# Kernel tuning notes

Hardware: AMD Instinct MI355X
Metric: run time of the kernel (lower is better)

## Reference

```python
import jax, jax.numpy as jnp
import numpy as np

B, N, C_IN, C_OUT, H_MLP, STEPS, DEG = 8, 128, 512, 512, 128, 10, 16
E = B * N * DEG  # edges per side


def _seg_mean(v, idx, n):
    s = jax.ops.segment_sum(v, idx, num_segments=n)
    c = jax.ops.segment_sum(jnp.ones((v.shape[0], 1), v.dtype), idx, num_segments=n)
    return s / jnp.maximum(c, 1.0)


def _relconv(x, ei, W1, W2, Wr, br):
    n = x.shape[0]
    src, dst = ei[0], ei[1]
    out1 = _seg_mean((x @ W1)[src], dst, n)  # flow source_to_target, mean aggr
    out2 = _seg_mean((x @ W2)[dst], src, n)  # flow target_to_source, mean aggr
    return x @ Wr + br + out1 + out2


def _gnn(x, ei, p):
    # GNNForEmbedding: 1 RelConv layer, LayerNorm(relu(.)), cat=True, lin=True (eval: dropout off)
    W1, W2, Wr, br, g, b, Fw, Fb = p
    h = jax.nn.relu(_relconv(x, ei, W1, W2, Wr, br))
    mu = h.mean(-1, keepdims=True)
    var = ((h - mu) ** 2).mean(-1, keepdims=True)
    h = (h - mu) / jnp.sqrt(var + 1e-5) * g + b
    return jnp.concatenate([x, h], -1) @ Fw + Fb


def setup_inputs():
    key = jax.random.key(0)
    ks = jax.random.split(key, 20)
    nn_ = B * N

    def randn(k, shape, s=1.0):
        return jax.random.normal(k, shape, jnp.float32) * s

    def mk_edges(k):
        k1, k2 = jax.random.split(k)
        off = jnp.repeat(jnp.arange(B, dtype=jnp.int32) * N, N * DEG)
        src = jax.random.randint(k1, (E,), 0, N, jnp.int32) + off
        dst = jax.random.randint(k2, (E,), 0, N, jnp.int32) + off
        return jnp.stack([src, dst])

    s = 0.04
    inp = {
        'x_s': randn(ks[0], (nn_, C_IN)),
        'edge_index_s': mk_edges(ks[1]),
        'edge_attr_s': randn(ks[2], (E, 1)),
        'batch_s': jnp.repeat(jnp.arange(B, dtype=jnp.int32), N),
        'x_t': randn(ks[3], (nn_, C_IN)),
        'edge_index_t': mk_edges(ks[4]),
        'edge_attr_t': randn(ks[5], (E, 1)),
        'batch_t': jnp.repeat(jnp.arange(B, dtype=jnp.int32), N),
        'e_lin1': randn(ks[6], (C_IN, C_OUT), s),
        'e_lin2': randn(ks[7], (C_IN, C_OUT), s),
        'e_rw': randn(ks[8], (C_IN, C_OUT), s),
        'e_rb': jnp.zeros((C_OUT,), jnp.float32),
        'e_g': jnp.ones((C_OUT,), jnp.float32),
        'e_b': jnp.zeros((C_OUT,), jnp.float32),
        'e_fw': randn(ks[9], (C_IN + C_OUT, C_OUT), s),
        'e_fb': jnp.zeros((C_OUT,), jnp.float32),
        'c_lin1': randn(ks[10], (C_IN, C_OUT), s),
        'c_lin2': randn(ks[11], (C_IN, C_OUT), s),
        'c_rw': randn(ks[12], (C_IN, C_OUT), s),
        'c_rb': jnp.zeros((C_OUT,), jnp.float32),
        'c_g': jnp.ones((C_OUT,), jnp.float32),
        'c_b': jnp.zeros((C_OUT,), jnp.float32),
        'c_fw': randn(ks[13], (C_IN + C_OUT, C_OUT), s),
        'c_fb': jnp.zeros((C_OUT,), jnp.float32),
        'm_w1': randn(ks[14], (C_OUT, H_MLP), s),
        'm_b1': jnp.zeros((H_MLP,), jnp.float32),
        'm_w2': randn(ks[15], (H_MLP,), s),
        'm_b2': jnp.zeros((), jnp.float32),
    }
    return inp


def reference(x_s, edge_index_s, edge_attr_s, batch_s, x_t, edge_index_t, edge_attr_t, batch_t,
              e_lin1, e_lin2, e_rw, e_rb, e_g, e_b, e_fw, e_fb,
              c_lin1, c_lin2, c_rw, c_rb, c_g, c_b, c_fw, c_fb,
              m_w1, m_b1, m_w2, m_b2):
    pe = (e_lin1, e_lin2, e_rw, e_rb, e_g, e_b, e_fw, e_fb)
    pc = (c_lin1, c_lin2, c_rw, c_rb, c_g, c_b, c_fw, c_fb)
    # embedding GNN (detached in original model)
    Hs = jax.lax.stop_gradient(_gnn(x_s, edge_index_s, pe)).reshape(B, N, C_OUT)
    Ht = jax.lax.stop_gradient(_gnn(x_t, edge_index_t, pe)).reshape(B, N, C_OUT)
    # all graphs have exactly N nodes -> masks are all-True, masked_softmax == softmax
    S_hat = jnp.einsum('bsc,btc->bst', Hs, Ht)
    S_0 = jax.nn.softmax(S_hat, axis=-1).reshape(B * N, N)
    rkey = jax.random.key(42)
    for t in range(STEPS):
        S = jax.nn.softmax(S_hat, axis=-1)
        R_s = jax.random.normal(jax.random.fold_in(rkey, t), (B, N, C_IN), jnp.float32)
        R_t = jnp.einsum('bst,bsc->btc', S, R_s)  # S^T @ R_s
        O_s = _gnn(R_s.reshape(-1, C_IN), edge_index_s, pc).reshape(B, N, C_OUT)
        O_t = _gnn(R_t.reshape(-1, C_IN), edge_index_t, pc).reshape(B, N, C_OUT)
        # fc1(O_s_i - O_t_j) = O_s_i@W1 - O_t_j@W1 + b1 (linearity): avoid O(Ns*Nt*C) diff tensor
        A = O_s @ m_w1 + m_b1          # [B, Ns, H]
        Bm = O_t @ m_w1                # [B, Nt, H]
        hid = jax.nn.relu(A[:, :, None, :] - Bm[:, None, :, :])  # [B, Ns, Nt, H]
        S_hat = S_hat + (hid @ m_w2 + m_b2)
    S_L = jax.nn.softmax(S_hat, axis=-1).reshape(B * N, N)
    return (S_0, S_L)
```

## Files before the change

### kernel.cpp

```cpp
#include <hip/hip_runtime.h>
#include <stdint.h>


typedef unsigned short u16;
typedef unsigned int u32;
typedef __attribute__((ext_vector_type(8))) short short8;
typedef __attribute__((ext_vector_type(4))) float f32x4;

__device__ inline u16 f2bf(float x) {
  u32 u = __float_as_uint(x);
  u32 r = (u + 0x7fffu + ((u >> 16) & 1u)) >> 16;
  return (u16)r;
}
__device__ inline float bf2f(u16 h) { return __uint_as_float(((u32)h) << 16); }
__device__ inline void split2(float x, u16& h, u16& l) {
  h = f2bf(x);
  l = f2bf(x - bf2f(h));
}

__host__ __device__ inline void tf2x32(uint32_t k0, uint32_t k1, uint32_t x0,
                                       uint32_t x1, uint32_t& o0, uint32_t& o1) {
  uint32_t ks0 = k0, ks1 = k1, ks2 = 0x1BD11BDAu ^ k0 ^ k1;
  x0 += ks0; x1 += ks1;
#define TF_R(r) { x0 += x1; x1 = (x1 << r) | (x1 >> (32 - r)); x1 ^= x0; }
  TF_R(13) TF_R(15) TF_R(26) TF_R(6)   x0 += ks1; x1 += ks2 + 1u;
  TF_R(17) TF_R(29) TF_R(16) TF_R(24)  x0 += ks2; x1 += ks0 + 2u;
  TF_R(13) TF_R(15) TF_R(26) TF_R(6)   x0 += ks0; x1 += ks1 + 3u;
  TF_R(17) TF_R(29) TF_R(16) TF_R(24)  x0 += ks1; x1 += ks2 + 4u;
  TF_R(13) TF_R(15) TF_R(26) TF_R(6)   x0 += ks2; x1 += ks0 + 5u;
#undef TF_R
  o0 = x0; o1 = x1;
}

__device__ inline float erfinv_f(float x) {
  float w = -log1pf(-x * x);
  float p;
  if (w < 5.0f) {
    w = w - 2.5f;
    p = 2.81022636e-08f;
    p = fmaf(p, w, 3.43273939e-07f);
    p = fmaf(p, w, -3.5233877e-06f);
    p = fmaf(p, w, -4.39150654e-06f);
    p = fmaf(p, w, 0.00021858087f);
    p = fmaf(p, w, -0.00125372503f);
    p = fmaf(p, w, -0.00417768164f);
    p = fmaf(p, w, 0.246640727f);
    p = fmaf(p, w, 1.50140941f);
  } else {
    w = sqrtf(w) - 3.0f;
    p = -0.000200214257f;
    p = fmaf(p, w, 0.000100950558f);
    p = fmaf(p, w, 0.00134934322f);
    p = fmaf(p, w, -0.00367342844f);
    p = fmaf(p, w, 0.00573950773f);
    p = fmaf(p, w, -0.0076224613f);
    p = fmaf(p, w, 0.00943887047f);
    p = fmaf(p, w, 1.00167406f);
    p = fmaf(p, w, 2.83297682f);
  }
  return p * x;
}

__device__ inline float bits_to_normal(uint32_t bits) {
  uint32_t fb = (bits >> 9) | 0x3f800000u;
  float f = __uint_as_float(fb) - 1.0f;
  float u = f * 2.0f + (-0.99999994f);
  u = fmaxf(-0.99999994f, u);
  return 1.41421356f * erfinv_f(u);
}

template <int OUTP, int BIASN, int BIASM, int AGGB>
__global__ __launch_bounds__(256) void mfma_gemm(
    int K,
    const u16* __restrict__ Ah, const u16* __restrict__ Al, int lda, int sA,
    const u16* __restrict__ Bh, const u16* __restrict__ Bl, int ldb, int sB,
    float* __restrict__ Cf, u16* __restrict__ Ch, u16* __restrict__ Cl,
    int ldc, int sC, const float* __restrict__ bias) {
  const int g = blockIdx.z;
  Ah += (size_t)g * sA; Al += (size_t)g * sA;
  Bh += (size_t)g * sB; Bl += (size_t)g * sB;
  if (OUTP) { Ch += (size_t)g * sC; Cl += (size_t)g * sC; }
  else { Cf += (size_t)g * sC; }
  __shared__ u16 As[2][64][64];
  __shared__ u16 Bs[2][64][64];
  const int tid = threadIdx.x;
  const int m0 = blockIdx.y * 64, n0 = blockIdx.x * 64;
  const int l = tid & 63;
  const int w = tid >> 6;
  const int wr = (w >> 1) * 32, wc = (w & 1) * 32;
  const int l15 = l & 15, lq = l >> 4;
  f32x4 acc[2][2] = {};
  const int sr = tid >> 3, sc = tid & 7;
  for (int k0 = 0; k0 < K; k0 += 64) {
    __syncthreads();
#pragma unroll
    for (int p = 0; p < 2; ++p) {
      int r = sr + p * 32;
      int dst = (sc ^ (r & 7)) * 8;
      *(uint4*)&As[0][r][dst] = *(const uint4*)&Ah[(size_t)(m0 + r) * lda + k0 + sc * 8];
      *(uint4*)&As[1][r][dst] = *(const uint4*)&Al[(size_t)(m0 + r) * lda + k0 + sc * 8];
      size_t boff;
      if (AGGB) {
        int rowg = (k0 < 128) ? (n0 + r) : (512 + n0 + r);
        boff = (size_t)rowg * ldb + (k0 & 127) + sc * 8;
      } else {
        boff = (size_t)(n0 + r) * ldb + k0 + sc * 8;
      }
      *(uint4*)&Bs[0][r][dst] = *(const uint4*)&Bh[boff];
      *(uint4*)&Bs[1][r][dst] = *(const uint4*)&Bl[boff];
    }
    __syncthreads();
#pragma unroll
    for (int kk = 0; kk < 2; ++kk) {
      short8 aH[2], aL[2], bH[2], bL[2];
#pragma unroll
      for (int i = 0; i < 2; ++i) {
        int mr = wr + i * 16 + l15;
        int ca = ((kk * 4 + lq) ^ (mr & 7)) * 8;
        aH[i] = *(const short8*)&As[0][mr][ca];
        aL[i] = *(const short8*)&As[1][mr][ca];
        int nr = wc + i * 16 + l15;
        int cb = ((kk * 4 + lq) ^ (nr & 7)) * 8;
        bH[i] = *(const short8*)&Bs[0][nr][cb];
        bL[i] = *(const short8*)&Bs[1][nr][cb];
      }
#pragma unroll
      for (int i = 0; i < 2; ++i)
#pragma unroll
        for (int j = 0; j < 2; ++j) {
          acc[i][j] = __builtin_amdgcn_mfma_f32_16x16x32_bf16(aH[i], bH[j], acc[i][j], 0, 0, 0);
          acc[i][j] = __builtin_amdgcn_mfma_f32_16x16x32_bf16(aL[i], bH[j], acc[i][j], 0, 0, 0);
          acc[i][j] = __builtin_amdgcn_mfma_f32_16x16x32_bf16(aH[i], bL[j], acc[i][j], 0, 0, 0);
        }
    }
  }
#pragma unroll
  for (int i = 0; i < 2; ++i)
#pragma unroll
    for (int j = 0; j < 2; ++j) {
      int n = n0 + wc + j * 16 + l15;
      int mb = m0 + wr + i * 16 + lq * 4;
      f32x4 v = acc[i][j];
      if (BIASN) {
        float b = bias[n];
        v[0] += b; v[1] += b; v[2] += b; v[3] += b;
      }
      if (BIASM) {
        f32x4 bb = *(const f32x4*)&bias[mb];
        v[0] += bb[0]; v[1] += bb[1]; v[2] += bb[2]; v[3] += bb[3];
      }
      if (OUTP) {
        u16 h[4], lo[4];
        split2(v[0], h[0], lo[0]); split2(v[1], h[1], lo[1]);
        split2(v[2], h[2], lo[2]); split2(v[3], h[3], lo[3]);
        uint2 hv = {(u32)h[0] | ((u32)h[1] << 16), (u32)h[2] | ((u32)h[3] << 16)};
        uint2 lv = {(u32)lo[0] | ((u32)lo[1] << 16), (u32)lo[2] | ((u32)lo[3] << 16)};
        *(uint2*)&Ch[(size_t)n * ldc + mb] = hv;
        *(uint2*)&Cl[(size_t)n * ldc + mb] = lv;
      } else {
        *(f32x4*)&Cf[(size_t)n * ldc + mb] = v;
      }
    }
}

__global__ __launch_bounds__(256) void count_kernel(const int* __restrict__ ei_s,
                                                    const int* __restrict__ ei_t,
                                                    int* __restrict__ Acnt,
                                                    int* __restrict__ degd,
                                                    int* __restrict__ degs) {
  int e = blockIdx.x * 256 + threadIdx.x;
  int side = e >> 14, idx = e & 16383;
  const int* ei = side ? ei_t : ei_s;
  int src = ei[idx], dst = ei[16384 + idx];
  int g = (dst >> 7) + side * 8;
  int dl = dst & 127, sl = src & 127;
  atomicAdd(&Acnt[(g * 128 + dl) * 128 + sl], 1);
  atomicAdd(&degd[g * 128 + dl], 1);
  atomicAdd(&degs[g * 128 + sl], 1);
}

__global__ __launch_bounds__(256) void norm_adj_kernel(const int* __restrict__ Acnt,
                                                       const int* __restrict__ degd,
                                                       const int* __restrict__ degs,
                                                       u16* __restrict__ Mh,
                                                       u16* __restrict__ Ml) {
  int idx = blockIdx.x * 256 + threadIdx.x;
  int g = idx >> 15, m = (idx >> 8) & 127, k = idx & 255;
  float val;
  if (k < 128)
    val = (float)Acnt[(g * 128 + m) * 128 + k] / (float)max(degd[g * 128 + m], 1);
  else
    val = (float)Acnt[(g * 128 + (k - 128)) * 128 + m] / (float)max(degs[g * 128 + m], 1);
  u16 h, lo;
  split2(val, h, lo);
  Mh[idx] = h; Ml[idx] = lo;
}

__global__ __launch_bounds__(256) void pack_kernel(const float* __restrict__ W1,
                                                   const float* __restrict__ W2,
                                                   const float* __restrict__ Wr,
                                                   float* __restrict__ Wcat) {
  int idx = blockIdx.x * 256 + threadIdx.x;
  int k = idx / 384, j4 = (idx % 384) * 4;
  float4 v;
  if (j4 < 512)       v = *(const float4*)&W1[k * 512 + j4];
  else if (j4 < 1024) v = *(const float4*)&W2[k * 512 + j4 - 512];
  else                v = *(const float4*)&Wr[k * 512 + j4 - 1024];
  *(float4*)&Wcat[k * 1536 + j4] = v;
}

__global__ __launch_bounds__(256) void convert_wT(const float* __restrict__ W,
                                                  u16* __restrict__ Th,
                                                  u16* __restrict__ Tl,
                                                  int K, int N) {
  int id = blockIdx.x * 256 + threadIdx.x;
  int k = id / N, n = id - k * N;
  u16 h, lo;
  split2(W[id], h, lo);
  Th[n * K + k] = h;
  Tl[n * K + k] = lo;
}

__global__ __launch_bounds__(128) void fbm_kernel(const float* __restrict__ fb,
                                                  const float* __restrict__ w1,
                                                  const float* __restrict__ b1,
                                                  float* __restrict__ fbm) {
  int h = threadIdx.x;
  float acc = b1[h];
  for (int c = 0; c < 512; ++c) acc = fmaf(fb[c], w1[c * 128 + h], acc);
  fbm[h] = acc;
}

__global__ __launch_bounds__(256) void copyx_kernel(const float* __restrict__ xs,
                                                    const float* __restrict__ xt,
                                                    u16* __restrict__ XHh,
                                                    u16* __restrict__ XHl) {
  int idx = blockIdx.x * 256 + threadIdx.x;
  int row = idx >> 7, c4 = (idx & 127) << 2;
  const float* src = (row < 1024) ? (xs + row * 512 + c4)
                                  : (xt + (row - 1024) * 512 + c4);
  float4 v = *(const float4*)src;
  u16 h[4], lo[4];
  split2(v.x, h[0], lo[0]); split2(v.y, h[1], lo[1]);
  split2(v.z, h[2], lo[2]); split2(v.w, h[3], lo[3]);
  uint2 hv = {(u32)h[0] | ((u32)h[1] << 16), (u32)h[2] | ((u32)h[3] << 16)};
  uint2 lv = {(u32)lo[0] | ((u32)lo[1] << 16), (u32)lo[2] | ((u32)lo[3] << 16)};
  *(uint2*)&XHh[row * 1024 + c4] = hv;
  *(uint2*)&XHl[row * 1024 + c4] = lv;
}

__global__ __launch_bounds__(256) void gemm_f32(
    int M, int N, int K,
    const float* __restrict__ A, int lda,
    const float* __restrict__ B, int ldb,
    float* __restrict__ C, int ldc) {
  int m0 = blockIdx.y * 64, n0 = blockIdx.x * 64;
  __shared__ float As[16][64];
  __shared__ float Bs[16][64];
  int tid = threadIdx.x;
  int tx = tid & 15, ty = tid >> 4;
  float acc[4][4] = {};
  for (int k0 = 0; k0 < K; k0 += 16) {
    {
      int m_l = tid & 63, k_l = (tid >> 6) << 2;
      float4 av = *(const float4*)&A[(m0 + m_l) * lda + k0 + k_l];
      As[k_l + 0][m_l] = av.x; As[k_l + 1][m_l] = av.y;
      As[k_l + 2][m_l] = av.z; As[k_l + 3][m_l] = av.w;
    }
    {
      int k_l = tid >> 4, n_l = (tid & 15) << 2;
      float4 bv = *(const float4*)&B[(k0 + k_l) * ldb + n0 + n_l];
      *(float4*)&Bs[k_l][n_l] = bv;
    }
    __syncthreads();
#pragma unroll
    for (int kk = 0; kk < 16; ++kk) {
      float4 a4 = *(const float4*)&As[kk][ty << 2];
      float4 b4 = *(const float4*)&Bs[kk][tx << 2];
      float av[4] = {a4.x, a4.y, a4.z, a4.w};
      float bv[4] = {b4.x, b4.y, b4.z, b4.w};
#pragma unroll
      for (int i = 0; i < 4; ++i)
#pragma unroll
        for (int j = 0; j < 4; ++j) acc[i][j] = fmaf(av[i], bv[j], acc[i][j]);
    }
    __syncthreads();
  }
#pragma unroll
  for (int i = 0; i < 4; ++i) {
    int m = m0 + (ty << 2) + i;
    float4 v = {acc[i][0], acc[i][1], acc[i][2], acc[i][3]};
    *(float4*)&C[m * ldc + n0 + (tx << 2)] = v;
  }
}

__global__ __launch_bounds__(256) void ln_stats(
    const u16* __restrict__ Yth, const u16* __restrict__ Ytl,
    const float* __restrict__ AGGt, const float* __restrict__ rb,
    float* __restrict__ partS, float* __restrict__ partQ) {
  int cg = blockIdx.x, ng = blockIdx.y;
  int lane = threadIdx.x & 63, cs = threadIdx.x >> 6;
  int node = ng * 64 + lane;
  float s = 0.f, q = 0.f;
#pragma unroll
  for (int k = 0; k < 16; ++k) {
    int c = cg * 64 + cs * 16 + k;
    size_t yi = (size_t)(1024 + c) * 2048 + node;
    float v = bf2f(Yth[yi]) + bf2f(Ytl[yi]) + rb[c] + AGGt[(size_t)c * 2048 + node];
    v = fmaxf(v, 0.f);
    s += v; q += v * v;
  }
  __shared__ float ls[4][64], lq[4][64];
  ls[cs][lane] = s; lq[cs][lane] = q;
  __syncthreads();
  if (cs == 0) {
    s = ls[0][lane] + ls[1][lane] + ls[2][lane] + ls[3][lane];
    q = lq[0][lane] + lq[1][lane] + lq[2][lane] + lq[3][lane];
    partS[cg * 2048 + node] = s;
    partQ[cg * 2048 + node] = q;
  }
}

__global__ __launch_bounds__(256) void ln_apply(
    const u16* __restrict__ Yth, const u16* __restrict__ Ytl,
    const float* __restrict__ AGGt, const float* __restrict__ partS,
    const float* __restrict__ partQ, const float* __restrict__ rb,
    const float* __restrict__ gam, const float* __restrict__ bet,
    u16* __restrict__ XHh, u16* __restrict__ XHl) {
  int cg = blockIdx.x, ng = blockIdx.y;
  int lane = threadIdx.x & 63, cs = threadIdx.x >> 6;
  int node = ng * 64 + lane;
  float s = 0.f, q = 0.f;
#pragma unroll
  for (int p = 0; p < 8; ++p) {
    s += partS[p * 2048 + node];
    q += partQ[p * 2048 + node];
  }
  float mu = s * (1.f / 512.f);
  float var = q * (1.f / 512.f) - mu * mu;
  float inv = 1.f / sqrtf(var + 1e-5f);
  __shared__ u16 oth[64][66], otl[64][66];
#pragma unroll
  for (int k = 0; k < 16; ++k) {
    int c = cg * 64 + cs * 16 + k;
    size_t yi = (size_t)(1024 + c) * 2048 + node;
    float v = bf2f(Yth[yi]) + bf2f(Ytl[yi]) + rb[c] + AGGt[(size_t)c * 2048 + node];
    v = fmaxf(v, 0.f);
    float o = (v - mu) * inv * gam[c] + bet[c];
    u16 h, lo;
    split2(o, h, lo);
    oth[lane][cs * 16 + k] = h;
    otl[lane][cs * 16 + k] = lo;
  }
  __syncthreads();
  int nl = threadIdx.x >> 2, cq = (threadIdx.x & 3) * 16;
  size_t xbase = (size_t)(ng * 64 + nl) * 1024 + 512 + cg * 64 + cq;
  uint4 h0, h1, l0, l1;
  h0 = *(const uint4*)&oth[nl][cq];     h1 = *(const uint4*)&oth[nl][cq + 8];
  l0 = *(const uint4*)&otl[nl][cq];     l1 = *(const uint4*)&otl[nl][cq + 8];
  *(uint4*)&XHh[xbase] = h0;  *(uint4*)&XHh[xbase + 8] = h1;
  *(uint4*)&XHl[xbase] = l0;  *(uint4*)&XHl[xbase + 8] = l1;
}

__global__ __launch_bounds__(256) void srk_kernel(
    const float* __restrict__ SH, u16* __restrict__ STh, u16* __restrict__ STl,
    u16* __restrict__ RsTh, u16* __restrict__ RsTl,
    u16* __restrict__ XHh, u16* __restrict__ XHl,
    float* __restrict__ outp, u32 k0, u32 k1) {
  int bid = blockIdx.x;
  int tid = threadIdx.x;
  if (bid < 512) {
    int r = bid * 2 + (tid >> 7);
    int t = tid & 127;
    int gg = r >> 7, s = r & 127;
    float a = SH[r * 128 + t];
    float m = a;
#pragma unroll
    for (int off = 32; off > 0; off >>= 1) m = fmaxf(m, __shfl_xor(m, off));
    __shared__ float red[2][4];
    int wv = tid >> 6;
    if ((tid & 63) == 0) red[0][wv] = m;
    __syncthreads();
    m = fmaxf(red[0][wv], red[0][wv ^ 1]);
    float e = expf(a - m);
    float su = e;
#pragma unroll
    for (int off = 32; off > 0; off >>= 1) su += __shfl_xor(su, off);
    if ((tid & 63) == 0) red[1][wv] = su;
    __syncthreads();
    su = red[1][wv] + red[1][wv ^ 1];
    float p = e / su;
    u16 h, lo;
    split2(p, h, lo);
    STh[(gg * 128 + t) * 128 + s] = h;
    STl[(gg * 128 + t) * 128 + s] = lo;
    if (outp) outp[r * 128 + t] = p;
  } else {
    u32 j = (u32)(bid - 512) * 256 + tid;
    u32 o0, o1;
    tf2x32(k0, k1, 0u, j, o0, o1);
    float val = bits_to_normal(o0 ^ o1);
    u32 node = j >> 9, ch = j & 511;
    u16 h, lo;
    split2(val, h, lo);
    XHh[node * 1024 + ch] = h;
    XHl[node * 1024 + ch] = lo;
    RsTh[ch * 1024 + node] = h;
    RsTl[ch * 1024 + node] = lo;
  }
}

__global__ __launch_bounds__(128) void dist_kernel(const float* __restrict__ Pt,
                                                   const float* __restrict__ b1,
                                                   const float* __restrict__ w2,
                                                   const float* __restrict__ b2,
                                                   float* __restrict__ SH) {
  int bs = blockIdx.x;
  int gb = bs >> 7;
  int t = threadIdx.x;
  __shared__ float arow[128], w2s[128];
  arow[t] = Pt[(size_t)t * 2048 + bs] + b1[t];
  w2s[t] = w2[t];
  __syncthreads();
  const float* pt = Pt + 1024 + gb * 128 + t;
  float acc = 0.f;
#pragma unroll 8
  for (int h = 0; h < 128; ++h) {
    float pv = pt[(size_t)h * 2048];
    acc += fmaxf(arow[h] - pv, 0.f) * w2s[h];
  }
  SH[bs * 128 + t] += acc + b2[0];
}

extern "C" void kernel_launch(void* const* d_in, const int* in_sizes, int n_in,
                              void* d_out, int out_size, void* d_ws, size_t ws_size,
                              hipStream_t stream) {
  const float* x_s = (const float*)d_in[0];
  const int* ei_s = (const int*)d_in[1];
  const float* x_t = (const float*)d_in[4];
  const int* ei_t = (const int*)d_in[5];
  const float* e_lin1 = (const float*)d_in[8];
  const float* e_lin2 = (const float*)d_in[9];
  const float* e_rw = (const float*)d_in[10];
  const float* e_rb = (const float*)d_in[11];
  const float* e_g = (const float*)d_in[12];
  const float* e_b = (const float*)d_in[13];
  const float* e_fw = (const float*)d_in[14];
  const float* e_fb = (const float*)d_in[15];
  const float* c_lin1 = (const float*)d_in[16];
  const float* c_lin2 = (const float*)d_in[17];
  const float* c_rw = (const float*)d_in[18];
  const float* c_rb = (const float*)d_in[19];
  const float* c_g = (const float*)d_in[20];
  const float* c_b = (const float*)d_in[21];
  const float* c_fw = (const float*)d_in[22];
  const float* c_fb = (const float*)d_in[23];
  const float* m_w1 = (const float*)d_in[24];
  const float* m_b1 = (const float*)d_in[25];
  const float* m_w2 = (const float*)d_in[26];
  const float* m_b2 = (const float*)d_in[27];
  float* out = (float*)d_out;
  float* ws = (float*)d_ws;

  u16* Mch   = (u16*)(ws + 0);
  u16* Mcl   = (u16*)(ws + 262144);
  u16* Yth   = (u16*)(ws + 524288);
  u16* Ytl   = (u16*)(ws + 2097152);
  float* AGGt = ws + 3670016;
  float* Pt   = AGGt;
  u16* XHh   = (u16*)(ws + 4718592);
  u16* XHl   = (u16*)(ws + 5767168);
  u16* WTeh  = (u16*)(ws + 6815744);
  u16* WTel  = (u16*)(ws + 7208960);
  u16* WTch  = (u16*)(ws + 7602176);
  u16* WTcl  = (u16*)(ws + 7995392);
  u16* FTeh  = (u16*)(ws + 8388608);
  u16* FTel  = (u16*)(ws + 8650752);
  u16* FmTh  = (u16*)(ws + 8912896);
  u16* FmTl  = (u16*)(ws + 8978432);
  u16* Oh    = (u16*)(ws + 9043968);
  u16* Ol    = (u16*)(ws + 9568256);
  u16* RsTh  = (u16*)(ws + 10092544);
  u16* RsTl  = (u16*)(ws + 10354688);
  u16* STh   = (u16*)(ws + 10616832);
  u16* STl   = (u16*)(ws + 10682368);
  float* SH  = ws + 10747904;
  float* Wstage = ws + 10878976;
  float* fbm = ws + 11665408;
  float* partS = ws + 11665536;
  float* partQ = ws + 11681920;
  int* Acnt  = (int*)Yth;
  int* degd  = Acnt + 262144;
  int* degs  = degd + 2048;

  hipMemsetAsync(Acnt, 0, (262144 + 4096) * sizeof(int), stream);
  count_kernel<<<128, 256, 0, stream>>>(ei_s, ei_t, Acnt, degd, degs);
  norm_adj_kernel<<<2048, 256, 0, stream>>>(Acnt, degd, degs, Mch, Mcl);
  pack_kernel<<<768, 256, 0, stream>>>(e_lin1, e_lin2, e_rw, Wstage);
  convert_wT<<<3072, 256, 0, stream>>>(Wstage, WTeh, WTel, 512, 1536);
  pack_kernel<<<768, 256, 0, stream>>>(c_lin1, c_lin2, c_rw, Wstage);
  convert_wT<<<3072, 256, 0, stream>>>(Wstage, WTch, WTcl, 512, 1536);
  convert_wT<<<2048, 256, 0, stream>>>(e_fw, FTeh, FTel, 1024, 512);
  gemm_f32<<<dim3(2, 16, 1), 256, 0, stream>>>(1024, 128, 512, c_fw, 512,
                                               m_w1, 128, Wstage, 128);
  convert_wT<<<512, 256, 0, stream>>>(Wstage, FmTh, FmTl, 1024, 128);
  fbm_kernel<<<1, 128, 0, stream>>>(c_fb, m_w1, m_b1, fbm);
  copyx_kernel<<<1024, 256, 0, stream>>>(x_s, x_t, XHh, XHl);

  auto relu_ln = [&](const float* rb, const float* g, const float* bb) {
    ln_stats<<<dim3(8, 32), 256, 0, stream>>>(Yth, Ytl, AGGt, rb, partS, partQ);
    ln_apply<<<dim3(8, 32), 256, 0, stream>>>(Yth, Ytl, AGGt, partS, partQ,
                                              rb, g, bb, XHh, XHl);
  };

  mfma_gemm<1, 0, 0, 0><<<dim3(24, 32, 1), 256, 0, stream>>>(
      512, XHh, XHl, 1024, 0, WTeh, WTel, 512, 0,
      nullptr, Yth, Ytl, 2048, 0, nullptr);
  mfma_gemm<0, 0, 0, 1><<<dim3(8, 2, 16), 256, 0, stream>>>(
      256, Mch, Mcl, 256, 32768, Yth, Ytl, 2048, 128,
      AGGt, nullptr, nullptr, 2048, 128, nullptr);
  relu_ln(e_rb, e_g, e_b);
  mfma_gemm<1, 0, 1, 0><<<dim3(32, 8, 1), 256, 0, stream>>>(
      1024, FTeh, FTel, 1024, 0, XHh, XHl, 1024, 0,
      nullptr, Oh, Ol, 512, 0, e_fb);
  mfma_gemm<0, 0, 0, 0><<<dim3(2, 2, 8), 256, 0, stream>>>(
      512, Oh + 1024 * 512, Ol + 1024 * 512, 512, 128 * 512,
      Oh, Ol, 512, 128 * 512,
      SH, nullptr, nullptr, 128, 16384, nullptr);

  for (int t = 0; t < 10; ++t) {
    uint32_t fk0, fk1;
    tf2x32(0u, 42u, 0u, (uint32_t)t, fk0, fk1);
    srk_kernel<<<2560, 256, 0, stream>>>(SH, STh, STl, RsTh, RsTl, XHh, XHl,
                                         (t == 0) ? out : nullptr, fk0, fk1);
    mfma_gemm<1, 0, 0, 0><<<dim3(2, 8, 8), 256, 0, stream>>>(
        128, RsTh, RsTl, 1024, 128, STh, STl, 128, 16384,
        nullptr, XHh + 1024 * 1024, XHl + 1024 * 1024, 1024, 128 * 1024, nullptr);
    mfma_gemm<1, 0, 0, 0><<<dim3(24, 32, 1), 256, 0, stream>>>(
        512, XHh, XHl, 1024, 0, WTch, WTcl, 512, 0,
        nullptr, Yth, Ytl, 2048, 0, nullptr);
    mfma_gemm<0, 0, 0, 1><<<dim3(8, 2, 16), 256, 0, stream>>>(
        256, Mch, Mcl, 256, 32768, Yth, Ytl, 2048, 128,
        AGGt, nullptr, nullptr, 2048, 128, nullptr);
    relu_ln(c_rb, c_g, c_b);
    mfma_gemm<0, 1, 0, 0><<<dim3(2, 32, 1), 256, 0, stream>>>(
        1024, XHh, XHl, 1024, 0, FmTh, FmTl, 1024, 0,
        Pt, nullptr, nullptr, 2048, 0, fbm);
    dist_kernel<<<1024, 128, 0, stream>>>(Pt, m_b1, m_w2, m_b2, SH);
  }
  srk_kernel<<<512, 256, 0, stream>>>(SH, STh, STl, RsTh, RsTl, XHh, XHl,
                                      out + 131072, 0u, 0u);
}
```

Measured before the change: 1.023 ms.

## Fuse distance update into softmax/RNG kernel and add 128x128 GEMM tile

Merges the per-step dist_kernel into the following softmax+RNG kernel so the S_hat update, softmax, transpose-split and next-step random generation run in one launch per iteration. This removes a launch and a round trip of SH through memory. It also adds a 512-thread 128x128-tile MFMA GEMM with XOR-swizzled LDS for the large weight GEMMs, giving more reuse per block but fewer blocks, which risks lower occupancy and less spread across CUs.

```diff
diff --git a/kernel.cpp b/kernel.cpp
--- a/kernel.cpp
+++ b/kernel.cpp
@@ -163,6 +163,84 @@
     }
 }
 
+template <int BIASM>
+__global__ __launch_bounds__(512) void mfma_gemm_big(
+    int K,
+    const u16* __restrict__ Ah, const u16* __restrict__ Al, int lda,
+    const u16* __restrict__ Bh, const u16* __restrict__ Bl, int ldb,
+    u16* __restrict__ Ch, u16* __restrict__ Cl, int ldc,
+    const float* __restrict__ bias) {
+  __shared__ u16 As[2][128][64];
+  __shared__ u16 Bs[2][128][64];
+  const int tid = threadIdx.x;
+  const int m0 = blockIdx.y * 128, n0 = blockIdx.x * 128;
+  const int l = tid & 63;
+  const int w = tid >> 6;
+  const int wm = (w >> 2) * 64;
+  const int wn = (w & 3) * 32;
+  const int l15 = l & 15, lq = l >> 4;
+  f32x4 acc[4][2] = {};
+  const int sr = tid >> 3, sc = tid & 7;
+  for (int k0 = 0; k0 < K; k0 += 64) {
+    __syncthreads();
+#pragma unroll
+    for (int p = 0; p < 2; ++p) {
+      int r = p * 64 + sr;
+      int dst = (sc ^ (r & 7)) * 8;
+      *(uint4*)&As[0][r][dst] = *(const uint4*)&Ah[(size_t)(m0 + r) * lda + k0 + sc * 8];
+      *(uint4*)&As[1][r][dst] = *(const uint4*)&Al[(size_t)(m0 + r) * lda + k0 + sc * 8];
+      *(uint4*)&Bs[0][r][dst] = *(const uint4*)&Bh[(size_t)(n0 + r) * ldb + k0 + sc * 8];
+      *(uint4*)&Bs[1][r][dst] = *(const uint4*)&Bl[(size_t)(n0 + r) * ldb + k0 + sc * 8];
+    }
+    __syncthreads();
+#pragma unroll
+    for (int kk = 0; kk < 2; ++kk) {
+      short8 aH[4], aL[4], bH[2], bL[2];
+#pragma unroll
+      for (int i = 0; i < 4; ++i) {
+        int mr = wm + i * 16 + l15;
+        int ca = ((kk * 4 + lq) ^ (mr & 7)) * 8;
+        aH[i] = *(const short8*)&As[0][mr][ca];
+        aL[i] = *(const short8*)&As[1][mr][ca];
+      }
+#pragma unroll
+      for (int j = 0; j < 2; ++j) {
+        int nr = wn + j * 16 + l15;
+        int cb = ((kk * 4 + lq) ^ (nr & 7)) * 8;
+        bH[j] = *(const short8*)&Bs[0][nr][cb];
+        bL[j] = *(const short8*)&Bs[1][nr][cb];
+      }
+#pragma unroll
+      for (int i = 0; i < 4; ++i)
+#pragma unroll
+        for (int j = 0; j < 2; ++j) {
+          acc[i][j] = __builtin_amdgcn_mfma_f32_16x16x32_bf16(aH[i], bH[j], acc[i][j], 0, 0, 0);
+          acc[i][j] = __builtin_amdgcn_mfma_f32_16x16x32_bf16(aL[i], bH[j], acc[i][j], 0, 0, 0);
+          acc[i][j] = __builtin_amdgcn_mfma_f32_16x16x32_bf16(aH[i], bL[j], acc[i][j], 0, 0, 0);
+        }
+    }
+  }
+#pragma unroll
+  for (int i = 0; i < 4; ++i)
+#pragma unroll
+    for (int j = 0; j < 2; ++j) {
+      int n = n0 + wn + j * 16 + l15;
+      int mb = m0 + wm + i * 16 + lq * 4;
+      f32x4 v = acc[i][j];
+      if (BIASM) {
+        f32x4 bb = *(const f32x4*)&bias[mb];
+        v[0] += bb[0]; v[1] += bb[1]; v[2] += bb[2]; v[3] += bb[3];
+      }
+      u16 h[4], lo[4];
+      split2(v[0], h[0], lo[0]); split2(v[1], h[1], lo[1]);
+      split2(v[2], h[2], lo[2]); split2(v[3], h[3], lo[3]);
+      uint2 hv = {(u32)h[0] | ((u32)h[1] << 16), (u32)h[2] | ((u32)h[3] << 16)};
+      uint2 lv = {(u32)lo[0] | ((u32)lo[1] << 16), (u32)lo[2] | ((u32)lo[3] << 16)};
+      *(uint2*)&Ch[(size_t)n * ldc + mb] = hv;
+      *(uint2*)&Cl[(size_t)n * ldc + mb] = lv;
+    }
+}
+
 __global__ __launch_bounds__(256) void count_kernel(const int* __restrict__ ei_s,
                                                     const int* __restrict__ ei_t,
                                                     int* __restrict__ Acnt,
@@ -362,40 +440,59 @@
   *(uint4*)&XHl[xbase] = l0;  *(uint4*)&XHl[xbase + 8] = l1;
 }
 
-__global__ __launch_bounds__(256) void srk_kernel(
-    const float* __restrict__ SH, u16* __restrict__ STh, u16* __restrict__ STl,
+__global__ __launch_bounds__(256) void tail_kernel(
+    float* __restrict__ SH, const float* __restrict__ Pt,
+    const float* __restrict__ b1, const float* __restrict__ w2,
+    const float* __restrict__ b2,
+    u16* __restrict__ STh, u16* __restrict__ STl,
     u16* __restrict__ RsTh, u16* __restrict__ RsTl,
     u16* __restrict__ XHh, u16* __restrict__ XHl,
-    float* __restrict__ outp, u32 k0, u32 k1) {
+    float* __restrict__ outp, int do_rng, u32 k0, u32 k1) {
   int bid = blockIdx.x;
   int tid = threadIdx.x;
   if (bid < 512) {
-    int r = bid * 2 + (tid >> 7);
+    int rl = tid >> 7;
     int t = tid & 127;
-    int gg = r >> 7, s = r & 127;
-    float a = SH[r * 128 + t];
-    float m = a;
+    int bs = bid * 2 + rl;
+    int gg = bs >> 7, s = bs & 127;
+    float val = SH[bs * 128 + t];
+    if (Pt) {
+      __shared__ float arow[2][128], w2s[128];
+      arow[rl][t] = Pt[(size_t)t * 2048 + bs] + b1[t];
+      if (tid < 128) w2s[tid] = w2[tid];
+      __syncthreads();
+      const float* pt = Pt + 1024 + gg * 128 + t;
+      float acc = 0.f;
+#pragma unroll 8
+      for (int h = 0; h < 128; ++h) {
+        float pv = pt[(size_t)h * 2048];
+        acc += fmaxf(arow[rl][h] - pv, 0.f) * w2s[h];
+      }
+      val += acc + b2[0];
+      SH[bs * 128 + t] = val;
+    }
+    float m = val;
 #pragma unroll
     for (int off = 32; off > 0; off >>= 1) m = fmaxf(m, __shfl_xor(m, off));
-    __shared__ float red[2][4];
+    __shared__ float redm[4], reds[4];
     int wv = tid >> 6;
-    if ((tid & 63) == 0) red[0][wv] = m;
-    __syncthreads();
-    m = fmaxf(red[0][wv], red[0][wv ^ 1]);
-    float e = expf(a - m);
+    if ((tid & 63) == 0) redm[wv] = m;
+    __syncthreads();
+    m = fmaxf(redm[wv], redm[wv ^ 1]);
+    float e = expf(val - m);
     float su = e;
 #pragma unroll
     for (int off = 32; off > 0; off >>= 1) su += __shfl_xor(su, off);
-    if ((tid & 63) == 0) red[1][wv] = su;
-    __syncthreads();
-    su = red[1][wv] + red[1][wv ^ 1];
+    if ((tid & 63) == 0) reds[wv] = su;
+    __syncthreads();
+    su = reds[wv] + reds[wv ^ 1];
     float p = e / su;
     u16 h, lo;
     split2(p, h, lo);
     STh[(gg * 128 + t) * 128 + s] = h;
     STl[(gg * 128 + t) * 128 + s] = lo;
-    if (outp) outp[r * 128 + t] = p;
-  } else {
+    if (outp) outp[bs * 128 + t] = p;
+  } else if (do_rng) {
     u32 j = (u32)(bid - 512) * 256 + tid;
     u32 o0, o1;
     tf2x32(k0, k1, 0u, j, o0, o1);
@@ -408,28 +505,6 @@
     RsTh[ch * 1024 + node] = h;
     RsTl[ch * 1024 + node] = lo;
   }
-}
-
-__global__ __launch_bounds__(128) void dist_kernel(const float* __restrict__ Pt,
-                                                   const float* __restrict__ b1,
-                                                   const float* __restrict__ w2,
-                                                   const float* __restrict__ b2,
-                                                   float* __restrict__ SH) {
-  int bs = blockIdx.x;
-  int gb = bs >> 7;
-  int t = threadIdx.x;
-  __shared__ float arow[128], w2s[128];
-  arow[t] = Pt[(size_t)t * 2048 + bs] + b1[t];
-  w2s[t] = w2[t];
-  __syncthreads();
-  const float* pt = Pt + 1024 + gb * 128 + t;
-  float acc = 0.f;
-#pragma unroll 8
-  for (int h = 0; h < 128; ++h) {
-    float pv = pt[(size_t)h * 2048];
-    acc += fmaxf(arow[h] - pv, 0.f) * w2s[h];
-  }
-  SH[bs * 128 + t] += acc + b2[0];
 }
 
 extern "C" void kernel_launch(void* const* d_in, const int* in_sizes, int n_in,
@@ -513,32 +588,33 @@
                                               rb, g, bb, XHh, XHl);
   };
 
-  mfma_gemm<1, 0, 0, 0><<<dim3(24, 32, 1), 256, 0, stream>>>(
-      512, XHh, XHl, 1024, 0, WTeh, WTel, 512, 0,
-      nullptr, Yth, Ytl, 2048, 0, nullptr);
+  mfma_gemm_big<0><<<dim3(12, 16), 512, 0, stream>>>(
+      512, XHh, XHl, 1024, WTeh, WTel, 512, Yth, Ytl, 2048, nullptr);
   mfma_gemm<0, 0, 0, 1><<<dim3(8, 2, 16), 256, 0, stream>>>(
       256, Mch, Mcl, 256, 32768, Yth, Ytl, 2048, 128,
       AGGt, nullptr, nullptr, 2048, 128, nullptr);
   relu_ln(e_rb, e_g, e_b);
-  mfma_gemm<1, 0, 1, 0><<<dim3(32, 8, 1), 256, 0, stream>>>(
-      1024, FTeh, FTel, 1024, 0, XHh, XHl, 1024, 0,
-      nullptr, Oh, Ol, 512, 0, e_fb);
+  mfma_gemm_big<1><<<dim3(16, 4), 512, 0, stream>>>(
+      1024, FTeh, FTel, 1024, XHh, XHl, 1024, Oh, Ol, 512, e_fb);
   mfma_gemm<0, 0, 0, 0><<<dim3(2, 2, 8), 256, 0, stream>>>(
       512, Oh + 1024 * 512, Ol + 1024 * 512, 512, 128 * 512,
       Oh, Ol, 512, 128 * 512,
       SH, nullptr, nullptr, 128, 16384, nullptr);
 
+  {
+    uint32_t fk0, fk1;
+    tf2x32(0u, 42u, 0u, 0u, fk0, fk1);
+    tail_kernel<<<2560, 256, 0, stream>>>(SH, nullptr, m_b1, m_w2, m_b2,
+                                          STh, STl, RsTh, RsTl, XHh, XHl,
+                                          out, 1, fk0, fk1);
+  }
+
   for (int t = 0; t < 10; ++t) {
-    uint32_t fk0, fk1;
-    tf2x32(0u, 42u, 0u, (uint32_t)t, fk0, fk1);
-    srk_kernel<<<2560, 256, 0, stream>>>(SH, STh, STl, RsTh, RsTl, XHh, XHl,
-                                         (t == 0) ? out : nullptr, fk0, fk1);
     mfma_gemm<1, 0, 0, 0><<<dim3(2, 8, 8), 256, 0, stream>>>(
         128, RsTh, RsTl, 1024, 128, STh, STl, 128, 16384,
         nullptr, XHh + 1024 * 1024, XHl + 1024 * 1024, 1024, 128 * 1024, nullptr);
-    mfma_gemm<1, 0, 0, 0><<<dim3(24, 32, 1), 256, 0, stream>>>(
-        512, XHh, XHl, 1024, 0, WTch, WTcl, 512, 0,
-        nullptr, Yth, Ytl, 2048, 0, nullptr);
+    mfma_gemm_big<0><<<dim3(12, 16), 512, 0, stream>>>(
+        512, XHh, XHl, 1024, WTch, WTcl, 512, Yth, Ytl, 2048, nullptr);
     mfma_gemm<0, 0, 0, 1><<<dim3(8, 2, 16), 256, 0, stream>>>(
         256, Mch, Mcl, 256, 32768, Yth, Ytl, 2048, 128,
         AGGt, nullptr, nullptr, 2048, 128, nullptr);
@@ -546,8 +622,11 @@
     mfma_gemm<0, 1, 0, 0><<<dim3(2, 32, 1), 256, 0, stream>>>(
         1024, XHh, XHl, 1024, 0, FmTh, FmTl, 1024, 0,
         Pt, nullptr, nullptr, 2048, 0, fbm);
-    dist_kernel<<<1024, 128, 0, stream>>>(Pt, m_b1, m_w2, m_b2, SH);
-  }
-  srk_kernel<<<512, 256, 0, stream>>>(SH, STh, STl, RsTh, RsTl, XHh, XHl,
-                                      out + 131072, 0u, 0u);
-}
+    uint32_t fk0, fk1;
+    tf2x32(0u, 42u, 0u, (uint32_t)(t + 1), fk0, fk1);
+    int do_rng = (t < 9) ? 1 : 0;
+    tail_kernel<<<do_rng ? 2560 : 512, 256, 0, stream>>>(
+        SH, Pt, m_b1, m_w2, m_b2, STh, STl, RsTh, RsTl, XHh, XHl,
+        (t == 9) ? (out + 131072) : nullptr, do_rng, fk0, fk1);
+  }
+}
```

New measurement: 1.040 ms. Within noise of the previous version (+1.7%).

## Reassociate S^T@R_s through weights and fold Fm projection into main GEMM

Applied to the files above, without the earlier changes.

The R_t = S^T R_s product is now applied after multiplying by the packed weights: R_s is projected through [W1|W2|Wr|Fm_top] once for all nodes, and the result for the target rows is obtained by multiplying S^T with the projected source features. This removes the transposed R_s copy and the separate K=1024 Fm GEMM, whose x-half is now extra output columns of the main GEMM and is added back through a new PADD epilogue. Weight packing and transposition are fused into one kernel, and the random-generation kernel is moved to the end of each iteration. The risk is that the main GEMM now covers only the source half plus extra columns, and the reassociated product changes rounding order slightly.

```diff
diff --git a/kernel.cpp b/kernel.cpp
--- a/kernel.cpp
+++ b/kernel.cpp
@@ -69,13 +69,14 @@
   return 1.41421356f * erfinv_f(u);
 }
 
-template <int OUTP, int BIASN, int BIASM, int AGGB>
+template <int OUTP, int BIASN, int BIASM, int AGGB, int PADD>
 __global__ __launch_bounds__(256) void mfma_gemm(
     int K,
     const u16* __restrict__ Ah, const u16* __restrict__ Al, int lda, int sA,
     const u16* __restrict__ Bh, const u16* __restrict__ Bl, int ldb, int sB,
     float* __restrict__ Cf, u16* __restrict__ Ch, u16* __restrict__ Cl,
-    int ldc, int sC, const float* __restrict__ bias) {
+    int ldc, int sC, const float* __restrict__ bias,
+    const u16* __restrict__ Padh, const u16* __restrict__ Padl) {
   const int g = blockIdx.z;
   Ah += (size_t)g * sA; Al += (size_t)g * sA;
   Bh += (size_t)g * sB; Bl += (size_t)g * sB;
@@ -149,6 +150,14 @@
         f32x4 bb = *(const f32x4*)&bias[mb];
         v[0] += bb[0]; v[1] += bb[1]; v[2] += bb[2]; v[3] += bb[3];
       }
+      if (PADD) {
+        uint2 ph = *(const uint2*)&Padh[(size_t)n * 2048 + mb];
+        uint2 pl = *(const uint2*)&Padl[(size_t)n * 2048 + mb];
+        v[0] += bf2f((u16)(ph.x & 0xffff)) + bf2f((u16)(pl.x & 0xffff));
+        v[1] += bf2f((u16)(ph.x >> 16)) + bf2f((u16)(pl.x >> 16));
+        v[2] += bf2f((u16)(ph.y & 0xffff)) + bf2f((u16)(pl.y & 0xffff));
+        v[3] += bf2f((u16)(ph.y >> 16)) + bf2f((u16)(pl.y >> 16));
+      }
       if (OUTP) {
         u16 h[4], lo[4];
         split2(v[0], h[0], lo[0]); split2(v[1], h[1], lo[1]);
@@ -196,17 +205,18 @@
   Mh[idx] = h; Ml[idx] = lo;
 }
 
-__global__ __launch_bounds__(256) void pack_kernel(const float* __restrict__ W1,
-                                                   const float* __restrict__ W2,
-                                                   const float* __restrict__ Wr,
-                                                   float* __restrict__ Wcat) {
-  int idx = blockIdx.x * 256 + threadIdx.x;
-  int k = idx / 384, j4 = (idx % 384) * 4;
-  float4 v;
-  if (j4 < 512)       v = *(const float4*)&W1[k * 512 + j4];
-  else if (j4 < 1024) v = *(const float4*)&W2[k * 512 + j4 - 512];
-  else                v = *(const float4*)&Wr[k * 512 + j4 - 1024];
-  *(float4*)&Wcat[k * 1536 + j4] = v;
+__global__ __launch_bounds__(256) void convert_packed(const float* __restrict__ W1,
+                                                      const float* __restrict__ W2,
+                                                      const float* __restrict__ Wr,
+                                                      u16* __restrict__ Th,
+                                                      u16* __restrict__ Tl) {
+  int id = blockIdx.x * 256 + threadIdx.x;
+  int n = id >> 9, k = id & 511;
+  const float* W = (n < 512) ? W1 : ((n < 1024) ? W2 : Wr);
+  float v = W[k * 512 + (n & 511)];
+  u16 h, lo;
+  split2(v, h, lo);
+  Th[id] = h; Tl[id] = lo;
 }
 
 __global__ __launch_bounds__(256) void convert_wT(const float* __restrict__ W,
@@ -219,6 +229,25 @@
   split2(W[id], h, lo);
   Th[n * K + k] = h;
   Tl[n * K + k] = lo;
+}
+
+__global__ __launch_bounds__(256) void fm_split(const float* __restrict__ Fm,
+                                                u16* __restrict__ WFTch,
+                                                u16* __restrict__ WFTcl,
+                                                u16* __restrict__ FmTrh,
+                                                u16* __restrict__ FmTrl) {
+  int id = blockIdx.x * 256 + threadIdx.x;
+  int k = id >> 7, h = id & 127;
+  float v = Fm[k * 128 + h];
+  u16 hi, lo;
+  split2(v, hi, lo);
+  if (k < 512) {
+    WFTch[(size_t)(1536 + h) * 512 + k] = hi;
+    WFTcl[(size_t)(1536 + h) * 512 + k] = lo;
+  } else {
+    FmTrh[(size_t)h * 512 + (k - 512)] = hi;
+    FmTrl[(size_t)h * 512 + (k - 512)] = lo;
+  }
 }
 
 __global__ __launch_bounds__(128) void fbm_kernel(const float* __restrict__ fb,
@@ -364,7 +393,6 @@
 
 __global__ __launch_bounds__(256) void srk_kernel(
     const float* __restrict__ SH, u16* __restrict__ STh, u16* __restrict__ STl,
-    u16* __restrict__ RsTh, u16* __restrict__ RsTl,
     u16* __restrict__ XHh, u16* __restrict__ XHl,
     float* __restrict__ outp, u32 k0, u32 k1) {
   int bid = blockIdx.x;
@@ -405,8 +433,6 @@
     split2(val, h, lo);
     XHh[node * 1024 + ch] = h;
     XHl[node * 1024 + ch] = lo;
-    RsTh[ch * 1024 + node] = h;
-    RsTl[ch * 1024 + node] = lo;
   }
 }
 
@@ -465,30 +491,28 @@
   u16* Mch   = (u16*)(ws + 0);
   u16* Mcl   = (u16*)(ws + 262144);
   u16* Yth   = (u16*)(ws + 524288);
-  u16* Ytl   = (u16*)(ws + 2097152);
-  float* AGGt = ws + 3670016;
-  float* Pt   = AGGt;
-  u16* XHh   = (u16*)(ws + 4718592);
-  u16* XHl   = (u16*)(ws + 5767168);
-  u16* WTeh  = (u16*)(ws + 6815744);
-  u16* WTel  = (u16*)(ws + 7208960);
-  u16* WTch  = (u16*)(ws + 7602176);
-  u16* WTcl  = (u16*)(ws + 7995392);
-  u16* FTeh  = (u16*)(ws + 8388608);
-  u16* FTel  = (u16*)(ws + 8650752);
-  u16* FmTh  = (u16*)(ws + 8912896);
-  u16* FmTl  = (u16*)(ws + 8978432);
-  u16* Oh    = (u16*)(ws + 9043968);
-  u16* Ol    = (u16*)(ws + 9568256);
-  u16* RsTh  = (u16*)(ws + 10092544);
-  u16* RsTl  = (u16*)(ws + 10354688);
-  u16* STh   = (u16*)(ws + 10616832);
-  u16* STl   = (u16*)(ws + 10682368);
-  float* SH  = ws + 10747904;
-  float* Wstage = ws + 10878976;
-  float* fbm = ws + 11665408;
-  float* partS = ws + 11665536;
-  float* partQ = ws + 11681920;
+  u16* Ytl   = (u16*)(ws + 2228224);
+  float* AGGt = ws + 3932160;
+  u16* XHh   = (u16*)(ws + 4980736);
+  u16* XHl   = (u16*)(ws + 6029312);
+  u16* WTeh  = (u16*)(ws + 7077888);
+  u16* WTel  = (u16*)(ws + 7471104);
+  u16* WFTch = (u16*)(ws + 7864320);
+  u16* WFTcl = (u16*)(ws + 8290304);
+  u16* FTeh  = (u16*)(ws + 8716288);
+  u16* FTel  = (u16*)(ws + 8978432);
+  u16* FmTrh = (u16*)(ws + 9240576);
+  u16* FmTrl = (u16*)(ws + 9273344);
+  u16* Oh    = (u16*)(ws + 9306112);
+  u16* Ol    = (u16*)(ws + 9830400);
+  u16* STh   = (u16*)(ws + 10354688);
+  u16* STl   = (u16*)(ws + 10420224);
+  float* SH  = ws + 10485760;
+  float* Pt  = ws + 10616832;
+  float* Fm  = ws + 10878976;
+  float* fbm = ws + 11010048;
+  float* partS = ws + 11010176;
+  float* partQ = ws + 11026560;
   int* Acnt  = (int*)Yth;
   int* degd  = Acnt + 262144;
   int* degs  = degd + 2048;
@@ -496,58 +520,59 @@
   hipMemsetAsync(Acnt, 0, (262144 + 4096) * sizeof(int), stream);
   count_kernel<<<128, 256, 0, stream>>>(ei_s, ei_t, Acnt, degd, degs);
   norm_adj_kernel<<<2048, 256, 0, stream>>>(Acnt, degd, degs, Mch, Mcl);
-  pack_kernel<<<768, 256, 0, stream>>>(e_lin1, e_lin2, e_rw, Wstage);
-  convert_wT<<<3072, 256, 0, stream>>>(Wstage, WTeh, WTel, 512, 1536);
-  pack_kernel<<<768, 256, 0, stream>>>(c_lin1, c_lin2, c_rw, Wstage);
-  convert_wT<<<3072, 256, 0, stream>>>(Wstage, WTch, WTcl, 512, 1536);
+  convert_packed<<<3072, 256, 0, stream>>>(e_lin1, e_lin2, e_rw, WTeh, WTel);
+  convert_packed<<<3072, 256, 0, stream>>>(c_lin1, c_lin2, c_rw, WFTch, WFTcl);
   convert_wT<<<2048, 256, 0, stream>>>(e_fw, FTeh, FTel, 1024, 512);
   gemm_f32<<<dim3(2, 16, 1), 256, 0, stream>>>(1024, 128, 512, c_fw, 512,
-                                               m_w1, 128, Wstage, 128);
-  convert_wT<<<512, 256, 0, stream>>>(Wstage, FmTh, FmTl, 1024, 128);
+                                               m_w1, 128, Fm, 128);
+  fm_split<<<512, 256, 0, stream>>>(Fm, WFTch, WFTcl, FmTrh, FmTrl);
   fbm_kernel<<<1, 128, 0, stream>>>(c_fb, m_w1, m_b1, fbm);
   copyx_kernel<<<1024, 256, 0, stream>>>(x_s, x_t, XHh, XHl);
 
-  auto relu_ln = [&](const float* rb, const float* g, const float* bb) {
-    ln_stats<<<dim3(8, 32), 256, 0, stream>>>(Yth, Ytl, AGGt, rb, partS, partQ);
-    ln_apply<<<dim3(8, 32), 256, 0, stream>>>(Yth, Ytl, AGGt, partS, partQ,
-                                              rb, g, bb, XHh, XHl);
-  };
-
-  mfma_gemm<1, 0, 0, 0><<<dim3(24, 32, 1), 256, 0, stream>>>(
+  mfma_gemm<1, 0, 0, 0, 0><<<dim3(24, 32, 1), 256, 0, stream>>>(
       512, XHh, XHl, 1024, 0, WTeh, WTel, 512, 0,
-      nullptr, Yth, Ytl, 2048, 0, nullptr);
-  mfma_gemm<0, 0, 0, 1><<<dim3(8, 2, 16), 256, 0, stream>>>(
+      nullptr, Yth, Ytl, 2048, 0, nullptr, nullptr, nullptr);
+  mfma_gemm<0, 0, 0, 1, 0><<<dim3(8, 2, 16), 256, 0, stream>>>(
       256, Mch, Mcl, 256, 32768, Yth, Ytl, 2048, 128,
-      AGGt, nullptr, nullptr, 2048, 128, nullptr);
-  relu_ln(e_rb, e_g, e_b);
-  mfma_gemm<1, 0, 1, 0><<<dim3(32, 8, 1), 256, 0, stream>>>(
+      AGGt, nullptr, nullptr, 2048, 128, nullptr, nullptr, nullptr);
+  ln_stats<<<dim3(8, 32), 256, 0, stream>>>(Yth, Ytl, AGGt, e_rb, partS, partQ);
+  ln_apply<<<dim3(8, 32), 256, 0, stream>>>(Yth, Ytl, AGGt, partS, partQ,
+                                            e_rb, e_g, e_b, XHh, XHl);
+  mfma_gemm<1, 0, 1, 0, 0><<<dim3(32, 8, 1), 256, 0, stream>>>(
       1024, FTeh, FTel, 1024, 0, XHh, XHl, 1024, 0,
-      nullptr, Oh, Ol, 512, 0, e_fb);
-  mfma_gemm<0, 0, 0, 0><<<dim3(2, 2, 8), 256, 0, stream>>>(
+      nullptr, Oh, Ol, 512, 0, e_fb, nullptr, nullptr);
+  mfma_gemm<0, 0, 0, 0, 0><<<dim3(2, 2, 8), 256, 0, stream>>>(
       512, Oh + 1024 * 512, Ol + 1024 * 512, 512, 128 * 512,
       Oh, Ol, 512, 128 * 512,
-      SH, nullptr, nullptr, 128, 16384, nullptr);
+      SH, nullptr, nullptr, 128, 16384, nullptr, nullptr, nullptr);
+
+  {
+    uint32_t fk0, fk1;
+    tf2x32(0u, 42u, 0u, 0u, fk0, fk1);
+    srk_kernel<<<2560, 256, 0, stream>>>(SH, STh, STl, XHh, XHl, out, fk0, fk1);
+  }
 
   for (int t = 0; t < 10; ++t) {
+    mfma_gemm<1, 0, 0, 0, 0><<<dim3(26, 16, 1), 256, 0, stream>>>(
+        512, XHh, XHl, 1024, 0, WFTch, WFTcl, 512, 0,
+        nullptr, Yth, Ytl, 2048, 0, nullptr, nullptr, nullptr);
+    mfma_gemm<1, 0, 0, 0, 0><<<dim3(26, 2, 8), 256, 0, stream>>>(
+        128, STh, STl, 128, 16384, Yth, Ytl, 2048, 128,
+        nullptr, Yth + 1024, Ytl + 1024, 2048, 128, nullptr, nullptr, nullptr);
+    mfma_gemm<0, 0, 0, 1, 0><<<dim3(8, 2, 16), 256, 0, stream>>>(
+        256, Mch, Mcl, 256, 32768, Yth, Ytl, 2048, 128,
+        AGGt, nullptr, nullptr, 2048, 128, nullptr, nullptr, nullptr);
+    ln_stats<<<dim3(8, 32), 256, 0, stream>>>(Yth, Ytl, AGGt, c_rb, partS, partQ);
+    ln_apply<<<dim3(8, 32), 256, 0, stream>>>(Yth, Ytl, AGGt, partS, partQ,
+                                              c_rb, c_g, c_b, XHh, XHl);
+    mfma_gemm<0, 1, 0, 0, 1><<<dim3(2, 32, 1), 256, 0, stream>>>(
+        512, XHh + 512, XHl + 512, 1024, 0, FmTrh, FmTrl, 512, 0,
+        Pt, nullptr, nullptr, 2048, 0, fbm,
+        Yth + (size_t)1536 * 2048, Ytl + (size_t)1536 * 2048);
+    dist_kernel<<<1024, 128, 0, stream>>>(Pt, m_b1, m_w2, m_b2, SH);
     uint32_t fk0, fk1;
-    tf2x32(0u, 42u, 0u, (uint32_t)t, fk0, fk1);
-    srk_kernel<<<2560, 256, 0, stream>>>(SH, STh, STl, RsTh, RsTl, XHh, XHl,
-                                         (t == 0) ? out : nullptr, fk0, fk1);
-    mfma_gemm<1, 0, 0, 0><<<dim3(2, 8, 8), 256, 0, stream>>>(
-        128, RsTh, RsTl, 1024, 128, STh, STl, 128, 16384,
-        nullptr, XHh + 1024 * 1024, XHl + 1024 * 1024, 1024, 128 * 1024, nullptr);
-    mfma_gemm<1, 0, 0, 0><<<dim3(24, 32, 1), 256, 0, stream>>>(
-        512, XHh, XHl, 1024, 0, WTch, WTcl, 512, 0,
-        nullptr, Yth, Ytl, 2048, 0, nullptr);
-    mfma_gemm<0, 0, 0, 1><<<dim3(8, 2, 16), 256, 0, stream>>>(
-        256, Mch, Mcl, 256, 32768, Yth, Ytl, 2048, 128,
-        AGGt, nullptr, nullptr, 2048, 128, nullptr);
-    relu_ln(c_rb, c_g, c_b);
-    mfma_gemm<0, 1, 0, 0><<<dim3(2, 32, 1), 256, 0, stream>>>(
-        1024, XHh, XHl, 1024, 0, FmTh, FmTl, 1024, 0,
-        Pt, nullptr, nullptr, 2048, 0, fbm);
-    dist_kernel<<<1024, 128, 0, stream>>>(Pt, m_b1, m_w2, m_b2, SH);
-  }
-  srk_kernel<<<512, 256, 0, stream>>>(SH, STh, STl, RsTh, RsTl, XHh, XHl,
-                                      out + 131072, 0u, 0u);
-}
+    tf2x32(0u, 42u, 0u, (uint32_t)(t + 1), fk0, fk1);
+    srk_kernel<<<(t < 9) ? 2560 : 512, 256, 0, stream>>>(
+        SH, STh, STl, XHh, XHl, (t == 9) ? (out + 131072) : nullptr, fk0, fk1);
+  }
+}
```

New measurement: 858.0 us. -16.1%, faster.
